# Performance work log

Measured on AMD Instinct MI355X. Metric: run time of the kernel, lower is better.

The kernel has to match this reference:

```python
import jax, jax.numpy as jnp
import numpy as np

MAX_LEN = 30
CONST_VAL = 0.0

def setup_inputs() -> dict:
    key = jax.random.key(0)
    k1, k2, k3 = jax.random.split(key, 3)
    B, T, F = 131072, 30, 10
    inputs = jax.random.normal(k1, (B, T, F), dtype=jnp.float32)
    w1 = jax.random.normal(k2, (1, MAX_LEN), dtype=jnp.float32) * 0.05
    w2 = jax.random.normal(k3, (1, MAX_LEN), dtype=jnp.float32) * 0.05
    return {"inputs": inputs, "w1": w1, "w2": w2}

def reference(inputs, w1, w2):
    B, T, F = inputs.shape  # T == 30 (hardcoded split count), F < MAX_LEN
    # matmul of (B,1,1) scalar with (1,max_len) == outer product -> (B, max_len)
    r1 = inputs[:, 0, 0][:, None] * w1[0]  # (B, 30)
    r2 = inputs[:, 0, 1][:, None] * w2[0]  # (B, 30)
    # concat along last dim then flatten rows, matching tf concat+reshape(-1,2)
    rc = jnp.stack([r1, r2], axis=-1).reshape(-1, 2)  # (N, 2), N = B*30
    N = rc.shape[0]
    K = (MAX_LEN - F) // 2  # number of shifted copies (original + K-1 shifts)
    # pad K-1 constant rows on top; shift i is rows [K-1-i : K-1-i+N] of padded
    pad = jnp.full((K - 1, 2), CONST_VAL, dtype=jnp.float32)
    P = jnp.concatenate([pad, rc], axis=0)  # (N+K-1, 2)
    shifts = jnp.stack(
        [jax.lax.dynamic_slice_in_dim(P, K - 1 - i, N, axis=0) for i in range(K)],
        axis=1,
    )  # (N, K, 2); shift-major column order matches tf.concat axis=1 order
    tens = shifts.reshape(N, 2 * K)  # (N, 2K)
    # tf.split(30, axis=0) + stack(axis=1): piece j row a = tens[j*B + a]
    tens = tens.reshape(30, B, 2 * K).transpose(1, 0, 2)  # (B, 30, 2K)
    return jnp.concatenate([tens, inputs[:, :, 2:]], axis=2)  # (B, 30, 2K+F-2)
```

## Files before the change

### kernel.cpp

```cpp
#include <hip/hip_runtime.h>


__global__ __launch_bounds__(256) void pack_kernel(const float* __restrict__ inp,
                                                   float2* __restrict__ xc, int B) {
    int q = blockIdx.x * blockDim.x + threadIdx.x;
    if (q < B) {
        const float* p = inp + (size_t)q * 300;
        xc[q] = make_float2(p[0], p[1]);
    }
}

#define ROWS 192

__global__ __launch_bounds__(ROWS) void main_kernel(
    const float* __restrict__ inp,
    const float2* __restrict__ xc,
    const float* __restrict__ w1,
    const float* __restrict__ w2,
    float* __restrict__ out,
    int B, int nrows) {
    __shared__ float w1s[30], w2s[30];
    __shared__ float lin[ROWS * 10];
    __shared__ float lout[ROWS * 29];

    int t = threadIdx.x;
    int base = blockIdx.x * ROWS;

    if (t < 30) w1s[t] = w1[t];
    else if (t >= 32 && t < 62) w2s[t - 32] = w2[t - 32];

    {
        const float4* gin = (const float4*)(inp + (size_t)base * 10);
        float4* l4 = (float4*)lin;
        const int nf4 = ROWS * 10 / 4;
        const int gcap = nrows * 10 / 4;
#pragma unroll
        for (int s = 0; s < (nf4 + ROWS - 1) / ROWS; ++s) {
            int idx = t + ROWS * s;
            if (idx < nf4 && base * 10 / 4 + idx < gcap) l4[idx] = gin[idx];
        }
    }
    __syncthreads();

    {
        int row = base + t;
        if (row >= nrows) row = nrows - 1;
        int b = row / 30;
        int j = row - b * 30;
        int m0 = j * B + b;
        int q0 = m0 / 30;
        int r0 = m0 - q0 * 30;

        float2 xa = xc[q0];
        float2 xb = (q0 >= 1) ? xc[q0 - 1] : make_float2(0.f, 0.f);

        float* lo = lout + t * 29;
#pragma unroll
        for (int i = 0; i < 10; ++i) {
            bool useA = (r0 >= i);
            float2 x = useA ? xa : xb;
            int r = useA ? (r0 - i) : (r0 - i + 30);
            bool valid = useA || (q0 >= 1);
            lo[2 * i]     = valid ? x.x * w1s[r] : 0.f;
            lo[2 * i + 1] = valid ? x.y * w2s[r] : 0.f;
        }
#pragma unroll
        for (int u = 0; u < 8; ++u) lo[20 + u] = lin[t * 10 + 2 + u];
    }
    __syncthreads();

    {
        float4* gout = (float4*)(out + (size_t)base * 28);
        const long long gcap = (long long)nrows * 7;
#pragma unroll
        for (int s = 0; s < 7; ++s) {
            int g = t + ROWS * s;
            int r = g / 7;
            int c4 = g - r * 7;
            const float* lp = lout + r * 29 + c4 * 4;
            if ((long long)base * 7 + g < gcap)
                gout[g] = make_float4(lp[0], lp[1], lp[2], lp[3]);
        }
    }
}

extern "C" void kernel_launch(void* const* d_in, const int* in_sizes, int n_in,
                              void* d_out, int out_size, void* d_ws, size_t ws_size,
                              hipStream_t stream) {
    const float* inp = (const float*)d_in[0];
    const float* w1  = (const float*)d_in[1];
    const float* w2  = (const float*)d_in[2];
    float* out = (float*)d_out;

    int B = in_sizes[0] / 300;
    int nrows = B * 30;

    float2* xc = (float2*)d_ws;

    pack_kernel<<<(B + 255) / 256, 256, 0, stream>>>(inp, xc, B);

    int grid = (nrows + ROWS - 1) / ROWS;
    main_kernel<<<grid, ROWS, 0, stream>>>(inp, xc, w1, w2, out, B, nrows);
}
```

Before: 557.2 us.

## Stage gathered xc values in LDS, load tail features directly, use nontemporal stores

The block size goes from 192 to 256 rows. Each block now preloads the few xc entries it needs (three neighbours per j) into shared memory, so threads no longer do their own scattered global gathers. The tail features are read directly into registers as float2 loads instead of being staged through a shared input tile. Output stores become nontemporal to avoid polluting the cache, at the cost of an extra index computation and relying on the qb-based neighbour indexing being correct.

```diff
diff --git a/kernel.cpp b/kernel.cpp
--- a/kernel.cpp
+++ b/kernel.cpp
@@ -1,5 +1,7 @@
 #include <hip/hip_runtime.h>
 
+
+typedef float f32x4 __attribute__((ext_vector_type(4)));
 
 __global__ __launch_bounds__(256) void pack_kernel(const float* __restrict__ inp,
                                                    float2* __restrict__ xc, int B) {
@@ -10,7 +12,7 @@
     }
 }
 
-#define ROWS 192
+#define ROWS 256
 
 __global__ __launch_bounds__(ROWS) void main_kernel(
     const float* __restrict__ inp,
@@ -20,39 +22,48 @@
     float* __restrict__ out,
     int B, int nrows) {
     __shared__ float w1s[30], w2s[30];
-    __shared__ float lin[ROWS * 10];
+    __shared__ float2 xq[30][3];
+    __shared__ int qb[30];
     __shared__ float lout[ROWS * 29];
 
     int t = threadIdx.x;
     int base = blockIdx.x * ROWS;
+    int b0 = base / 30;
 
-    if (t < 30) w1s[t] = w1[t];
-    else if (t >= 32 && t < 62) w2s[t - 32] = w2[t - 32];
+    int row = base + t;
+    int rowc = (row < nrows) ? row : (nrows - 1);
 
-    {
-        const float4* gin = (const float4*)(inp + (size_t)base * 10);
-        float4* l4 = (float4*)lin;
-        const int nf4 = ROWS * 10 / 4;
-        const int gcap = nrows * 10 / 4;
-#pragma unroll
-        for (int s = 0; s < (nf4 + ROWS - 1) / ROWS; ++s) {
-            int idx = t + ROWS * s;
-            if (idx < nf4 && base * 10 / 4 + idx < gcap) l4[idx] = gin[idx];
-        }
+    const float2* tin = (const float2*)(inp + (size_t)rowc * 10 + 2);
+    float2 t0 = tin[0];
+    float2 t1 = tin[1];
+    float2 t2 = tin[2];
+    float2 t3 = tin[3];
+
+    if (t < 90) {
+        int jj = t / 3;
+        int dq = t - jj * 3;
+        int qbase = (jj * B + b0) / 30;
+        int q = qbase + dq - 1;
+        float2 v = (q >= 0 && q < B) ? xc[q] : make_float2(0.f, 0.f);
+        xq[jj][dq] = v;
+        if (dq == 1) qb[jj] = qbase;
+    } else if (t >= 96 && t < 126) {
+        w1s[t - 96] = w1[t - 96];
+    } else if (t >= 128 && t < 158) {
+        w2s[t - 128] = w2[t - 128];
     }
     __syncthreads();
 
     {
-        int row = base + t;
-        if (row >= nrows) row = nrows - 1;
-        int b = row / 30;
-        int j = row - b * 30;
+        int b = rowc / 30;
+        int j = rowc - b * 30;
         int m0 = j * B + b;
         int q0 = m0 / 30;
         int r0 = m0 - q0 * 30;
 
-        float2 xa = xc[q0];
-        float2 xb = (q0 >= 1) ? xc[q0 - 1] : make_float2(0.f, 0.f);
+        int ia = q0 - qb[j] + 1;
+        float2 xa = xq[j][ia];
+        float2 xb = xq[j][ia - 1];
 
         float* lo = lout + t * 29;
 #pragma unroll
@@ -60,17 +71,17 @@
             bool useA = (r0 >= i);
             float2 x = useA ? xa : xb;
             int r = useA ? (r0 - i) : (r0 - i + 30);
-            bool valid = useA || (q0 >= 1);
+            bool valid = (m0 - i) >= 0;
             lo[2 * i]     = valid ? x.x * w1s[r] : 0.f;
             lo[2 * i + 1] = valid ? x.y * w2s[r] : 0.f;
         }
-#pragma unroll
-        for (int u = 0; u < 8; ++u) lo[20 + u] = lin[t * 10 + 2 + u];
+        lo[20] = t0.x; lo[21] = t0.y; lo[22] = t1.x; lo[23] = t1.y;
+        lo[24] = t2.x; lo[25] = t2.y; lo[26] = t3.x; lo[27] = t3.y;
     }
     __syncthreads();
 
     {
-        float4* gout = (float4*)(out + (size_t)base * 28);
+        f32x4* gout = (f32x4*)(out + (size_t)base * 28);
         const long long gcap = (long long)nrows * 7;
 #pragma unroll
         for (int s = 0; s < 7; ++s) {
@@ -78,8 +89,10 @@
             int r = g / 7;
             int c4 = g - r * 7;
             const float* lp = lout + r * 29 + c4 * 4;
-            if ((long long)base * 7 + g < gcap)
-                gout[g] = make_float4(lp[0], lp[1], lp[2], lp[3]);
+            if ((long long)base * 7 + g < gcap) {
+                f32x4 v = {lp[0], lp[1], lp[2], lp[3]};
+                __builtin_nontemporal_store(v, &gout[g]);
+            }
         }
     }
 }
```

New measurement: 544.7 us. 1.02x faster.

## Drop LDS staging and write output rows directly with two threads per row

Applied to the files above, without the earlier changes.

Removes the shared-memory staging of input and output tiles. Each output row is now split between two threads: one computes the first 14 shifted products, the other computes the remaining 6 and copies the 8 passthrough input features, and both store straight to global with vector stores. This cuts LDS traffic and the barrier between compute and store. In exchange, global loads and stores are strided by row (112-byte rows), so coalescing is worse than the previous contiguous tile copy, and the validity check changes from q0>=1 to m0-i>=0.

```diff
diff --git a/kernel.cpp b/kernel.cpp
--- a/kernel.cpp
+++ b/kernel.cpp
@@ -1,5 +1,8 @@
 #include <hip/hip_runtime.h>
 
+
+typedef float f32x4 __attribute__((ext_vector_type(4)));
+typedef float f32x2 __attribute__((ext_vector_type(2)));
 
 __global__ __launch_bounds__(256) void pack_kernel(const float* __restrict__ inp,
                                                    float2* __restrict__ xc, int B) {
@@ -10,9 +13,7 @@
     }
 }
 
-#define ROWS 192
-
-__global__ __launch_bounds__(ROWS) void main_kernel(
+__global__ __launch_bounds__(256) void main_kernel(
     const float* __restrict__ inp,
     const float2* __restrict__ xc,
     const float* __restrict__ w1,
@@ -20,67 +21,63 @@
     float* __restrict__ out,
     int B, int nrows) {
     __shared__ float w1s[30], w2s[30];
-    __shared__ float lin[ROWS * 10];
-    __shared__ float lout[ROWS * 29];
-
     int t = threadIdx.x;
-    int base = blockIdx.x * ROWS;
-
     if (t < 30) w1s[t] = w1[t];
     else if (t >= 32 && t < 62) w2s[t - 32] = w2[t - 32];
-
-    {
-        const float4* gin = (const float4*)(inp + (size_t)base * 10);
-        float4* l4 = (float4*)lin;
-        const int nf4 = ROWS * 10 / 4;
-        const int gcap = nrows * 10 / 4;
-#pragma unroll
-        for (int s = 0; s < (nf4 + ROWS - 1) / ROWS; ++s) {
-            int idx = t + ROWS * s;
-            if (idx < nf4 && base * 10 / 4 + idx < gcap) l4[idx] = gin[idx];
-        }
-    }
     __syncthreads();
 
-    {
-        int row = base + t;
-        if (row >= nrows) row = nrows - 1;
-        int b = row / 30;
-        int j = row - b * 30;
-        int m0 = j * B + b;
-        int q0 = m0 / 30;
-        int r0 = m0 - q0 * 30;
+    int pairid = t >> 1;
+    int h = t & 1;
+    int row = blockIdx.x * 128 + pairid;
+    if (row >= nrows) return;
 
-        float2 xa = xc[q0];
-        float2 xb = (q0 >= 1) ? xc[q0 - 1] : make_float2(0.f, 0.f);
+    int b = row / 30;
+    int j = row - b * 30;
+    int m0 = j * B + b;
+    int q0 = m0 / 30;
+    int r0 = m0 - q0 * 30;
 
-        float* lo = lout + t * 29;
+    float2 xa = xc[q0];
+    float2 xb = (q0 >= 1) ? xc[q0 - 1] : make_float2(0.f, 0.f);
+
+    float* orow = out + (size_t)row * 28;
+
+    if (h == 0) {
+        float f[14];
 #pragma unroll
-        for (int i = 0; i < 10; ++i) {
+        for (int k = 0; k < 14; ++k) {
+            int i = k >> 1, c = k & 1;
             bool useA = (r0 >= i);
-            float2 x = useA ? xa : xb;
             int r = useA ? (r0 - i) : (r0 - i + 30);
-            bool valid = useA || (q0 >= 1);
-            lo[2 * i]     = valid ? x.x * w1s[r] : 0.f;
-            lo[2 * i + 1] = valid ? x.y * w2s[r] : 0.f;
+            float x = c ? (useA ? xa.y : xb.y) : (useA ? xa.x : xb.x);
+            float w = c ? w2s[r] : w1s[r];
+            f[k] = (m0 - i >= 0) ? x * w : 0.f;
         }
+        *(f32x4*)(orow + 0)  = (f32x4){f[0], f[1], f[2], f[3]};
+        *(f32x4*)(orow + 4)  = (f32x4){f[4], f[5], f[6], f[7]};
+        *(f32x4*)(orow + 8)  = (f32x4){f[8], f[9], f[10], f[11]};
+        *(f32x2*)(orow + 12) = (f32x2){f[12], f[13]};
+    } else {
+        const float* irow = inp + (size_t)row * 10;
+        f32x2 a0 = *(const f32x2*)(irow + 2);
+        f32x2 a1 = *(const f32x2*)(irow + 4);
+        f32x2 a2 = *(const f32x2*)(irow + 6);
+        f32x2 a3 = *(const f32x2*)(irow + 8);
+
+        float f[6];
 #pragma unroll
-        for (int u = 0; u < 8; ++u) lo[20 + u] = lin[t * 10 + 2 + u];
-    }
-    __syncthreads();
-
-    {
-        float4* gout = (float4*)(out + (size_t)base * 28);
-        const long long gcap = (long long)nrows * 7;
-#pragma unroll
-        for (int s = 0; s < 7; ++s) {
-            int g = t + ROWS * s;
-            int r = g / 7;
-            int c4 = g - r * 7;
-            const float* lp = lout + r * 29 + c4 * 4;
-            if ((long long)base * 7 + g < gcap)
-                gout[g] = make_float4(lp[0], lp[1], lp[2], lp[3]);
+        for (int k = 14; k < 20; ++k) {
+            int i = k >> 1, c = k & 1;
+            bool useA = (r0 >= i);
+            int r = useA ? (r0 - i) : (r0 - i + 30);
+            float x = c ? (useA ? xa.y : xb.y) : (useA ? xa.x : xb.x);
+            float w = c ? w2s[r] : w1s[r];
+            f[k - 14] = (m0 - i >= 0) ? x * w : 0.f;
         }
+        *(f32x2*)(orow + 14) = (f32x2){f[0], f[1]};
+        *(f32x4*)(orow + 16) = (f32x4){f[2], f[3], f[4], f[5]};
+        *(f32x4*)(orow + 20) = (f32x4){a0.x, a0.y, a1.x, a1.y};
+        *(f32x4*)(orow + 24) = (f32x4){a2.x, a2.y, a3.x, a3.y};
     }
 }
 
@@ -99,6 +96,6 @@
 
     pack_kernel<<<(B + 255) / 256, 256, 0, stream>>>(inp, xc, B);
 
-    int grid = (nrows + ROWS - 1) / ROWS;
-    main_kernel<<<grid, ROWS, 0, stream>>>(inp, xc, w1, w2, out, B, nrows);
+    int grid = (nrows + 127) / 128;
+    main_kernel<<<grid, 256, 0, stream>>>(inp, xc, w1, w2, out, B, nrows);
 }
```

New measurement: 628.8 us. 12.9% more time.
